# Performance work log

Hardware: AMD Instinct MI355X
Metric: run time of the kernel (lower is better)

The kernel has to match this reference:

```python
import jax, jax.numpy as jnp
import numpy as np

N, T, D, H = 64, 512, 512, 512


def setup_inputs() -> dict:
    key = jax.random.key(0)
    k1, k2, k3, k4 = jax.random.split(key, 4)
    x = jax.random.normal(k1, (N, T, D), dtype=jnp.float32)
    h0 = jax.random.normal(k2, (N, H), dtype=jnp.float32)
    Wx = jax.random.normal(k3, (D, H), dtype=jnp.float32) / jnp.sqrt(jnp.float32(D))
    Wh = jax.random.normal(k4, (H, H), dtype=jnp.float32) / jnp.sqrt(jnp.float32(H))
    b = jnp.zeros((H,), dtype=jnp.float32)
    return {"x": x, "h0": h0, "Wx": Wx, "Wh": Wh, "b": b}


def reference(x, h0, Wx, Wh, b):
    # Precompute the input-to-hidden projection for all timesteps at once
    # (one big GEMM), then scan the sequential hidden-state recurrence.
    xWx = jnp.einsum('ntd,dh->nth', x, Wx) + b  # (N, T, H)

    def step(h_prev, xw_t):
        h_next = jnp.tanh(xw_t + h_prev @ Wh)  # (N, H)
        return h_next, h_next

    # scan over time: move T to leading axis
    _, h_seq = jax.lax.scan(step, h0, jnp.swapaxes(xWx, 0, 1))  # (T, N, H)
    return jnp.swapaxes(h_seq, 0, 1)  # (N, T, H)
```

## Files before the change

kernel.cpp:

```cpp
#include <hip/hip_runtime.h>
#include <hip/hip_bf16.h>
#include <cmath>


#define DH     512
#define NSEQ   64
#define TSTEPS 512
#define MTOT   32768

typedef float v2f __attribute__((ext_vector_type(2)));

__global__ __launch_bounds__(256) void xw_gemm(
    const float* __restrict__ X,
    const float* __restrict__ Wx,
    const float* __restrict__ b,
    float* __restrict__ XW)
{
    __shared__ float As[16][64];
    __shared__ float Bs[16][64];

    const int bm = blockIdx.x * 64;
    const int bn = blockIdx.y * 64;
    const int tid = threadIdx.x;
    const int tr = tid >> 4;
    const int tc = tid & 15;

    float acc[4][4] = {};

    for (int k0 = 0; k0 < DH; k0 += 16) {
        {
            int m  = tid >> 2;
            int kk = (tid & 3) * 4;
            const float4 v = *(const float4*)&X[(size_t)(bm + m) * DH + k0 + kk];
            As[kk + 0][m] = v.x; As[kk + 1][m] = v.y;
            As[kk + 2][m] = v.z; As[kk + 3][m] = v.w;
        }
        {
            int k  = tid >> 4;
            int j4 = (tid & 15) * 4;
            *(float4*)&Bs[k][j4] = *(const float4*)&Wx[(size_t)(k0 + k) * DH + bn + j4];
        }
        __syncthreads();

        #pragma unroll
        for (int k = 0; k < 16; ++k) {
            float a0 = As[k][tr * 4 + 0], a1 = As[k][tr * 4 + 1];
            float a2 = As[k][tr * 4 + 2], a3 = As[k][tr * 4 + 3];
            float b0 = Bs[k][tc * 4 + 0], b1 = Bs[k][tc * 4 + 1];
            float b2 = Bs[k][tc * 4 + 2], b3 = Bs[k][tc * 4 + 3];
            acc[0][0] += a0 * b0; acc[0][1] += a0 * b1; acc[0][2] += a0 * b2; acc[0][3] += a0 * b3;
            acc[1][0] += a1 * b0; acc[1][1] += a1 * b1; acc[1][2] += a1 * b2; acc[1][3] += a1 * b3;
            acc[2][0] += a2 * b0; acc[2][1] += a2 * b1; acc[2][2] += a2 * b2; acc[2][3] += a2 * b3;
            acc[3][0] += a3 * b0; acc[3][1] += a3 * b1; acc[3][2] += a3 * b2; acc[3][3] += a3 * b3;
        }
        __syncthreads();
    }

    #pragma unroll
    for (int i = 0; i < 4; ++i) {
        const size_t row = (size_t)(bm + tr * 4 + i);
        #pragma unroll
        for (int j = 0; j < 4; ++j) {
            const int col = bn + tc * 4 + j;
            XW[row * DH + col] = acc[i][j] + b[col];
        }
    }
}

__global__ __launch_bounds__(512, 2) void rnn_rec5(
    const float* __restrict__ Wh,
    const float* __restrict__ h0,
    float* __restrict__ out,
    unsigned long long* __restrict__ hbuf)
{
    __shared__ float hslice[8][64];
    __shared__ float partb[2][8][128];

    const int bid  = blockIdx.x;
    const int xcd  = bid & 7;
    const int idx  = bid >> 3;
    const int seq  = xcd * 8 + (idx & 7);
    const int part = idx >> 3;
    const int tid  = threadIdx.x;
    const int lane = tid & 63;
    const int s    = tid >> 6;
    const int colbase = part * 128;
    const int c0   = colbase + lane * 2;

    v2f wv[64];
    #pragma unroll
    for (int k = 0; k < 64; ++k)
        wv[k] = *(const v2f*)&Wh[(size_t)(s * 64 + k) * DH + c0];
    #pragma unroll
    for (int k = 0; k < 64; ++k)
        asm volatile("" : "+v"(wv[k]));

    const int rwave = s - 2 * part;
    const bool is_reducer = (rwave == 0) | (rwave == 1);
    const int q     = rwave * 64 + lane;
    const int mycol = colbase + q;
    const int slot  = s * 64 + lane;

    hslice[s][lane] = h0[(size_t)seq * DH + slot];

    float* __restrict__ outn = out + (size_t)seq * TSTEPS * DH;
    float xw_cur = is_reducer ? outn[mycol] : 0.0f;

    for (int t = 0; t < TSTEPS; ++t) {
        const int buf = t & 1;

        v2f acc = {0.0f, 0.0f};
        #pragma unroll
        for (int qq = 0; qq < 16; ++qq) {
            const float4 h4 = *(const float4*)&hslice[s][qq * 4];
            v2f hb;
            hb.x = h4.x; hb.y = h4.x; acc = __builtin_elementwise_fma(hb, wv[4*qq+0], acc);
            hb.x = h4.y; hb.y = h4.y; acc = __builtin_elementwise_fma(hb, wv[4*qq+1], acc);
            hb.x = h4.z; hb.y = h4.z; acc = __builtin_elementwise_fma(hb, wv[4*qq+2], acc);
            hb.x = h4.w; hb.y = h4.w; acc = __builtin_elementwise_fma(hb, wv[4*qq+3], acc);
        }
        *(v2f*)&partb[buf][s][lane * 2] = acc;
        __syncthreads();

        unsigned long long* hb64 = &hbuf[((size_t)buf * NSEQ + seq) * DH];
        if (is_reducer) {
            float ssum = partb[buf][0][q] + partb[buf][1][q]
                       + partb[buf][2][q] + partb[buf][3][q]
                       + partb[buf][4][q] + partb[buf][5][q]
                       + partb[buf][6][q] + partb[buf][7][q];
            const float hval = tanhf(xw_cur + ssum);
            if (t < TSTEPS - 1) {
                const unsigned long long v =
                    ((unsigned long long)(unsigned)(t + 1) << 32) |
                    (unsigned long long)__float_as_uint(hval);
                __hip_atomic_store(&hb64[mycol], v,
                                   __ATOMIC_RELAXED, __HIP_MEMORY_SCOPE_AGENT);
            }
            hslice[s][lane] = hval;
            outn[(size_t)t * DH + mycol] = hval;
            if (t < TSTEPS - 1)
                xw_cur = outn[(size_t)(t + 1) * DH + mycol];
        } else if (t < TSTEPS - 1) {
            unsigned long long v;
            do {
                v = __hip_atomic_load(&hb64[slot], __ATOMIC_RELAXED,
                                      __HIP_MEMORY_SCOPE_AGENT);
            } while ((unsigned)(v >> 32) < (unsigned)(t + 1));
            hslice[s][lane] = __uint_as_float((unsigned)v);
        }
    }
}

__global__ __launch_bounds__(1024) void rnn_rec(
    const float* __restrict__ Wh,
    const float* __restrict__ h0,
    float* __restrict__ out)
{
    __shared__ float hsh[DH];
    __shared__ float part[8][DH];

    const int n     = blockIdx.x;
    const int tid   = threadIdx.x;
    const int jgrp  = tid & 127;
    const int ks    = tid >> 7;
    const int kbase = ks * 64;

    if (tid < DH) hsh[tid] = h0[(size_t)n * DH + tid];
    __syncthreads();

    const float4* __restrict__ Wh4 = (const float4*)Wh;
    float* __restrict__ outn = out + (size_t)n * TSTEPS * DH;

    float xw_cur = (tid < DH) ? outn[tid] : 0.0f;

    for (int t = 0; t < TSTEPS; ++t) {
        float xw_next = 0.0f;
        if (tid < DH && t < TSTEPS - 1) xw_next = outn[(size_t)(t + 1) * DH + tid];

        float4 acc = {0.0f, 0.0f, 0.0f, 0.0f};
        #pragma unroll 8
        for (int k = 0; k < 64; ++k) {
            const float hk = hsh[kbase + k];
            const float4 w = Wh4[(size_t)(kbase + k) * 128 + jgrp];
            acc.x += hk * w.x; acc.y += hk * w.y;
            acc.z += hk * w.z; acc.w += hk * w.w;
        }
        *(float4*)&part[ks][jgrp * 4] = acc;
        __syncthreads();

        if (tid < DH) {
            const int j = tid;
            float sum = part[0][j] + part[1][j] + part[2][j] + part[3][j]
                      + part[4][j] + part[5][j] + part[6][j] + part[7][j];
            const float hv = tanhf(xw_cur + sum);
            hsh[j] = hv;
            outn[(size_t)t * DH + j] = hv;
            xw_cur = xw_next;
        }
        __syncthreads();
    }
}

extern "C" void kernel_launch(void* const* d_in, const int* in_sizes, int n_in,
                              void* d_out, int out_size, void* d_ws, size_t ws_size,
                              hipStream_t stream) {
    const float* x  = (const float*)d_in[0];
    const float* h0 = (const float*)d_in[1];
    const float* Wx = (const float*)d_in[2];
    const float* Wh = (const float*)d_in[3];
    const float* b  = (const float*)d_in[4];
    float* out = (float*)d_out;

    xw_gemm<<<dim3(MTOT / 64, DH / 64), 256, 0, stream>>>(x, Wx, b, out);

    const size_t hbuf_bytes = (size_t)2 * NSEQ * DH * sizeof(unsigned long long);
    if (ws_size >= hbuf_bytes) {
        unsigned long long* hbuf = (unsigned long long*)d_ws;
        hipMemsetAsync(hbuf, 0, hbuf_bytes, stream);
        rnn_rec5<<<256, 512, 0, stream>>>(Wh, h0, out, hbuf);
    } else {
        rnn_rec<<<NSEQ, 1024, 0, stream>>>(Wh, h0, out);
    }
}
```

Measured before the change: 890.8 us.

## Interleave two sequences per block to hide cross-block hidden-state exchange latency

Each block now handles two sequences (a column quarter of each) instead of one, halving the grid to 128 blocks. The two sequences' steps are interleaved, and the polling load for one sequence's exchanged hidden state is issued before the other sequence's matvec runs, so global-memory exchange latency overlaps with compute. The block-to-sequence mapping also drops the XCD-aware grouping, so the blocks exchanging data for a sequence may no longer share an XCD. That can raise cross-die atomic latency, and two barriers per step add serialization.

```diff
diff --git a/kernel.cpp b/kernel.cpp
--- a/kernel.cpp
+++ b/kernel.cpp
@@ -67,20 +67,20 @@
     }
 }
 
-__global__ __launch_bounds__(512, 2) void rnn_rec5(
+__global__ __launch_bounds__(512, 2) void rnn_rec7(
     const float* __restrict__ Wh,
     const float* __restrict__ h0,
     float* __restrict__ out,
     unsigned long long* __restrict__ hbuf)
 {
-    __shared__ float hslice[8][64];
+    __shared__ float hslice[2][8][64];
     __shared__ float partb[2][8][128];
 
     const int bid  = blockIdx.x;
-    const int xcd  = bid & 7;
-    const int idx  = bid >> 3;
-    const int seq  = xcd * 8 + (idx & 7);
-    const int part = idx >> 3;
+    const int part = bid & 3;
+    const int g    = bid >> 2;
+    const int seq0 = g * 2;
+    const int seq1 = seq0 + 1;
     const int tid  = threadIdx.x;
     const int lane = tid & 63;
     const int s    = tid >> 6;
@@ -101,52 +101,113 @@
     const int mycol = colbase + q;
     const int slot  = s * 64 + lane;
 
-    hslice[s][lane] = h0[(size_t)seq * DH + slot];
-
-    float* __restrict__ outn = out + (size_t)seq * TSTEPS * DH;
-    float xw_cur = is_reducer ? outn[mycol] : 0.0f;
+    hslice[0][s][lane] = h0[(size_t)seq0 * DH + slot];
+    hslice[1][s][lane] = h0[(size_t)seq1 * DH + slot];
+
+    float* __restrict__ o0 = out + (size_t)seq0 * TSTEPS * DH;
+    float* __restrict__ o1 = out + (size_t)seq1 * TSTEPS * DH;
+    float xw0 = is_reducer ? o0[mycol] : 0.0f;
+    float xw1 = is_reducer ? o1[mycol] : 0.0f;
+
+    unsigned long long* const b0s0 = &hbuf[((size_t)0 * NSEQ + seq0) * DH];
+    unsigned long long* const b1s0 = &hbuf[((size_t)1 * NSEQ + seq0) * DH];
+    unsigned long long* const b0s1 = &hbuf[((size_t)0 * NSEQ + seq1) * DH];
+    unsigned long long* const b1s1 = &hbuf[((size_t)1 * NSEQ + seq1) * DH];
+
+    unsigned long long pf0 = 0, pf1 = 0;
+    __syncthreads();
 
     for (int t = 0; t < TSTEPS; ++t) {
         const int buf = t & 1;
-
-        v2f acc = {0.0f, 0.0f};
-        #pragma unroll
-        for (int qq = 0; qq < 16; ++qq) {
-            const float4 h4 = *(const float4*)&hslice[s][qq * 4];
-            v2f hb;
-            hb.x = h4.x; hb.y = h4.x; acc = __builtin_elementwise_fma(hb, wv[4*qq+0], acc);
-            hb.x = h4.y; hb.y = h4.y; acc = __builtin_elementwise_fma(hb, wv[4*qq+1], acc);
-            hb.x = h4.z; hb.y = h4.z; acc = __builtin_elementwise_fma(hb, wv[4*qq+2], acc);
-            hb.x = h4.w; hb.y = h4.w; acc = __builtin_elementwise_fma(hb, wv[4*qq+3], acc);
-        }
-        *(v2f*)&partb[buf][s][lane * 2] = acc;
-        __syncthreads();
-
-        unsigned long long* hb64 = &hbuf[((size_t)buf * NSEQ + seq) * DH];
+        const unsigned wantP = (unsigned)t;
+        unsigned long long* const pb0 = buf ? b0s0 : b1s0;
+        unsigned long long* const pb1 = buf ? b0s1 : b1s1;
+        unsigned long long* const cb0 = buf ? b1s0 : b0s0;
+        unsigned long long* const cb1 = buf ? b1s1 : b0s1;
+
+        if (t > 0 && !is_reducer) {
+            pf1 = __hip_atomic_load(&pb1[slot], __ATOMIC_RELAXED,
+                                    __HIP_MEMORY_SCOPE_AGENT);
+            unsigned long long v = pf0;
+            while ((unsigned)(v >> 32) < wantP)
+                v = __hip_atomic_load(&pb0[slot], __ATOMIC_RELAXED,
+                                      __HIP_MEMORY_SCOPE_AGENT);
+            hslice[0][s][lane] = __uint_as_float((unsigned)v);
+        }
+
+        {
+            v2f acc = {0.0f, 0.0f};
+            #pragma unroll
+            for (int qq = 0; qq < 16; ++qq) {
+                const float4 h4 = *(const float4*)&hslice[0][s][qq * 4];
+                v2f hb;
+                hb.x = h4.x; hb.y = h4.x; acc = __builtin_elementwise_fma(hb, wv[4*qq+0], acc);
+                hb.x = h4.y; hb.y = h4.y; acc = __builtin_elementwise_fma(hb, wv[4*qq+1], acc);
+                hb.x = h4.z; hb.y = h4.z; acc = __builtin_elementwise_fma(hb, wv[4*qq+2], acc);
+                hb.x = h4.w; hb.y = h4.w; acc = __builtin_elementwise_fma(hb, wv[4*qq+3], acc);
+            }
+            *(v2f*)&partb[0][s][lane * 2] = acc;
+        }
+        __syncthreads();
+
         if (is_reducer) {
-            float ssum = partb[buf][0][q] + partb[buf][1][q]
-                       + partb[buf][2][q] + partb[buf][3][q]
-                       + partb[buf][4][q] + partb[buf][5][q]
-                       + partb[buf][6][q] + partb[buf][7][q];
-            const float hval = tanhf(xw_cur + ssum);
+            float ssum = partb[0][0][q] + partb[0][1][q] + partb[0][2][q] + partb[0][3][q]
+                       + partb[0][4][q] + partb[0][5][q] + partb[0][6][q] + partb[0][7][q];
+            const float hv = tanhf(xw0 + ssum);
             if (t < TSTEPS - 1) {
                 const unsigned long long v =
                     ((unsigned long long)(unsigned)(t + 1) << 32) |
-                    (unsigned long long)__float_as_uint(hval);
-                __hip_atomic_store(&hb64[mycol], v,
+                    (unsigned long long)__float_as_uint(hv);
+                __hip_atomic_store(&cb0[mycol], v,
                                    __ATOMIC_RELAXED, __HIP_MEMORY_SCOPE_AGENT);
             }
-            hslice[s][lane] = hval;
-            outn[(size_t)t * DH + mycol] = hval;
+            hslice[0][s][lane] = hv;
+            o0[(size_t)t * DH + mycol] = hv;
             if (t < TSTEPS - 1)
-                xw_cur = outn[(size_t)(t + 1) * DH + mycol];
+                xw0 = o0[(size_t)(t + 1) * DH + mycol];
         } else if (t < TSTEPS - 1) {
-            unsigned long long v;
-            do {
-                v = __hip_atomic_load(&hb64[slot], __ATOMIC_RELAXED,
+            pf0 = __hip_atomic_load(&cb0[slot], __ATOMIC_RELAXED,
+                                    __HIP_MEMORY_SCOPE_AGENT);
+        }
+
+        if (t > 0 && !is_reducer) {
+            unsigned long long v = pf1;
+            while ((unsigned)(v >> 32) < wantP)
+                v = __hip_atomic_load(&pb1[slot], __ATOMIC_RELAXED,
                                       __HIP_MEMORY_SCOPE_AGENT);
-            } while ((unsigned)(v >> 32) < (unsigned)(t + 1));
-            hslice[s][lane] = __uint_as_float((unsigned)v);
+            hslice[1][s][lane] = __uint_as_float((unsigned)v);
+        }
+
+        {
+            v2f acc = {0.0f, 0.0f};
+            #pragma unroll
+            for (int qq = 0; qq < 16; ++qq) {
+                const float4 h4 = *(const float4*)&hslice[1][s][qq * 4];
+                v2f hb;
+                hb.x = h4.x; hb.y = h4.x; acc = __builtin_elementwise_fma(hb, wv[4*qq+0], acc);
+                hb.x = h4.y; hb.y = h4.y; acc = __builtin_elementwise_fma(hb, wv[4*qq+1], acc);
+                hb.x = h4.z; hb.y = h4.z; acc = __builtin_elementwise_fma(hb, wv[4*qq+2], acc);
+                hb.x = h4.w; hb.y = h4.w; acc = __builtin_elementwise_fma(hb, wv[4*qq+3], acc);
+            }
+            *(v2f*)&partb[1][s][lane * 2] = acc;
+        }
+        __syncthreads();
+
+        if (is_reducer) {
+            float ssum = partb[1][0][q] + partb[1][1][q] + partb[1][2][q] + partb[1][3][q]
+                       + partb[1][4][q] + partb[1][5][q] + partb[1][6][q] + partb[1][7][q];
+            const float hv = tanhf(xw1 + ssum);
+            if (t < TSTEPS - 1) {
+                const unsigned long long v =
+                    ((unsigned long long)(unsigned)(t + 1) << 32) |
+                    (unsigned long long)__float_as_uint(hv);
+                __hip_atomic_store(&cb1[mycol], v,
+                                   __ATOMIC_RELAXED, __HIP_MEMORY_SCOPE_AGENT);
+            }
+            hslice[1][s][lane] = hv;
+            o1[(size_t)t * DH + mycol] = hv;
+            if (t < TSTEPS - 1)
+                xw1 = o1[(size_t)(t + 1) * DH + mycol];
         }
     }
 }
@@ -217,7 +278,7 @@
     if (ws_size >= hbuf_bytes) {
         unsigned long long* hbuf = (unsigned long long*)d_ws;
         hipMemsetAsync(hbuf, 0, hbuf_bytes, stream);
-        rnn_rec5<<<256, 512, 0, stream>>>(Wh, h0, out, hbuf);
+        rnn_rec7<<<128, 512, 0, stream>>>(Wh, h0, out, hbuf);
     } else {
         rnn_rec<<<NSEQ, 1024, 0, stream>>>(Wh, h0, out);
     }
```

After: 1.340 ms. 50.5% more time.

## Split recurrence by K-slices with per-column owner reduction via global flags

Applied to the files above, without the earlier changes.

Adds a new recurrent kernel in which each of the four blocks per sequence holds a 128-row K-slice of Wh in registers and computes a partial dot product for all 512 columns. Non-owner threads publish their partials through tagged 64-bit atomic slots, and the owning block spins on three slots, sums them, applies tanh and stores its 128-element h piece. Compared with the previous kernel, each block now needs only its own h slice plus three remote partials per column, removing the full-h broadcast and the cross-wave LDS reduction. The cost is three polled global loads per owner thread per step and a workspace three times larger. It is used when the workspace is large enough, and the older kernels stay as fallbacks.

```diff
diff --git a/kernel.cpp b/kernel.cpp
--- a/kernel.cpp
+++ b/kernel.cpp
@@ -67,6 +67,96 @@
     }
 }
 
+__global__ __launch_bounds__(512, 2) void rnn_rec9(
+    const float* __restrict__ Wh,
+    const float* __restrict__ h0,
+    float* __restrict__ out,
+    unsigned long long* __restrict__ hbuf)
+{
+    __shared__ float hpiece[2][128];
+
+    const int bid  = blockIdx.x;
+    const int xcd  = bid & 7;
+    const int idx  = bid >> 3;
+    const int seq  = xcd * 8 + (idx & 7);
+    const int part = idx >> 3;
+    const int tid  = threadIdx.x;
+    const int kbase = part * 128;
+
+    float wv[128];
+    #pragma unroll
+    for (int kk = 0; kk < 128; ++kk)
+        wv[kk] = Wh[(size_t)(kbase + kk) * DH + tid];
+    #pragma unroll
+    for (int kk = 0; kk < 128; ++kk)
+        asm volatile("" : "+v"(wv[kk]));
+
+    const int  pj       = tid >> 7;
+    const bool is_owner = (pj == part);
+    const int  isl      = part - (part > pj ? 1 : 0);
+
+    if (tid < 128) hpiece[0][tid] = h0[(size_t)seq * DH + kbase + tid];
+
+    float* __restrict__ outn = out + (size_t)seq * TSTEPS * DH;
+    float xw_cur    = is_owner ? outn[tid] : 0.0f;
+    float hval_prev = 0.0f;
+
+    unsigned long long* const sb0 = hbuf + ((size_t)(0 * NSEQ + seq) * DH + tid) * 3;
+    unsigned long long* const sb1 = hbuf + ((size_t)(1 * NSEQ + seq) * DH + tid) * 3;
+
+    __syncthreads();
+
+    for (int t = 0; t < TSTEPS; ++t) {
+        const int buf = t & 1;
+        const float* hp = hpiece[buf];
+
+        float a0 = 0.0f, a1 = 0.0f, a2 = 0.0f, a3 = 0.0f;
+        #pragma unroll
+        for (int kk = 0; kk < 128; kk += 4) {
+            const float4 h4 = *(const float4*)&hp[kk];
+            a0 = fmaf(h4.x, wv[kk + 0], a0);
+            a1 = fmaf(h4.y, wv[kk + 1], a1);
+            a2 = fmaf(h4.z, wv[kk + 2], a2);
+            a3 = fmaf(h4.w, wv[kk + 3], a3);
+        }
+        const float contrib = (a0 + a1) + (a2 + a3);
+
+        unsigned long long* const sb = buf ? sb1 : sb0;
+        const unsigned want = (unsigned)(t + 1);
+
+        if (!is_owner) {
+            const unsigned long long v =
+                ((unsigned long long)want << 32) |
+                (unsigned long long)__float_as_uint(contrib);
+            __hip_atomic_store(sb + isl, v, __ATOMIC_RELAXED,
+                               __HIP_MEMORY_SCOPE_AGENT);
+        } else {
+            if (t > 0) outn[(size_t)(t - 1) * DH + tid] = hval_prev;
+            float xw_next = (t < TSTEPS - 1) ? outn[(size_t)(t + 1) * DH + tid]
+                                             : 0.0f;
+            unsigned long long v0, v1, v2;
+            do {
+                v0 = __hip_atomic_load(sb + 0, __ATOMIC_RELAXED,
+                                       __HIP_MEMORY_SCOPE_AGENT);
+                v1 = __hip_atomic_load(sb + 1, __ATOMIC_RELAXED,
+                                       __HIP_MEMORY_SCOPE_AGENT);
+                v2 = __hip_atomic_load(sb + 2, __ATOMIC_RELAXED,
+                                       __HIP_MEMORY_SCOPE_AGENT);
+            } while ((unsigned)(v0 >> 32) < want ||
+                     (unsigned)(v1 >> 32) < want ||
+                     (unsigned)(v2 >> 32) < want);
+            const float z = xw_cur
+                + ((contrib + __uint_as_float((unsigned)v0))
+                 + (__uint_as_float((unsigned)v1) + __uint_as_float((unsigned)v2)));
+            hval_prev = tanhf(z);
+            hpiece[buf ^ 1][tid & 127] = hval_prev;
+            xw_cur = xw_next;
+        }
+        __syncthreads();
+    }
+    if (is_owner) outn[(size_t)(TSTEPS - 1) * DH + tid] = hval_prev;
+}
+
 __global__ __launch_bounds__(512, 2) void rnn_rec5(
     const float* __restrict__ Wh,
     const float* __restrict__ h0,
@@ -108,7 +198,6 @@
 
     for (int t = 0; t < TSTEPS; ++t) {
         const int buf = t & 1;
-
         v2f acc = {0.0f, 0.0f};
         #pragma unroll
         for (int qq = 0; qq < 16; ++qq) {
@@ -213,10 +302,15 @@
 
     xw_gemm<<<dim3(MTOT / 64, DH / 64), 256, 0, stream>>>(x, Wx, b, out);
 
-    const size_t hbuf_bytes = (size_t)2 * NSEQ * DH * sizeof(unsigned long long);
-    if (ws_size >= hbuf_bytes) {
+    const size_t rec9_bytes = (size_t)2 * NSEQ * DH * 3 * sizeof(unsigned long long);
+    const size_t rec5_bytes = (size_t)2 * NSEQ * DH * sizeof(unsigned long long);
+    if (ws_size >= rec9_bytes) {
         unsigned long long* hbuf = (unsigned long long*)d_ws;
-        hipMemsetAsync(hbuf, 0, hbuf_bytes, stream);
+        hipMemsetAsync(hbuf, 0, rec9_bytes, stream);
+        rnn_rec9<<<256, 512, 0, stream>>>(Wh, h0, out, hbuf);
+    } else if (ws_size >= rec5_bytes) {
+        unsigned long long* hbuf = (unsigned long long*)d_ws;
+        hipMemsetAsync(hbuf, 0, rec5_bytes, stream);
         rnn_rec5<<<256, 512, 0, stream>>>(Wh, h0, out, hbuf);
     } else {
         rnn_rec<<<NSEQ, 1024, 0, stream>>>(Wh, h0, out);
```

Result: slower. 1.683 ms (+88.9%).

## Fuse input projection GEMM into recurrent kernel, computing xW tiles during spin-waits

Applied to the files above, without the earlier changes.

Removes the separate xw_gemm launch when workspace is available. The recurrent kernel now computes the x·Wx projection for its own sequence and column slice in 64-timestep tiles held in shared memory, one 8-wide k-chunk per recurrence step, while waiting for peers' hidden states. This is meant to hide GEMM work in the latency-bound recurrence and to avoid writing and re-reading the projection through global memory. In exchange it adds shared memory, register pressure and extra work on the per-step critical path, which could lengthen each step.

```diff
diff --git a/kernel.cpp b/kernel.cpp
--- a/kernel.cpp
+++ b/kernel.cpp
@@ -10,71 +10,49 @@
 
 typedef float v2f __attribute__((ext_vector_type(2)));
 
-__global__ __launch_bounds__(256) void xw_gemm(
+#define GEMM_CHUNK(SB)                                                         \
+    {                                                                          \
+        float2 w2[8];                                                          \
+        _Pragma("unroll")                                                      \
+        for (int kk = 0; kk < 8; ++kk)                                         \
+            w2[kk] = *(const float2*)&wstage[SB][kk][gc * 2];                  \
+        _Pragma("unroll")                                                      \
+        for (int r = 0; r < 8; ++r) {                                          \
+            const float4 xa = *(const float4*)&xstage[SB][rg * 8 + r][0];      \
+            const float4 xb = *(const float4*)&xstage[SB][rg * 8 + r][4];      \
+            accg[r][0] = fmaf(xa.x, w2[0].x, accg[r][0]);                      \
+            accg[r][1] = fmaf(xa.x, w2[0].y, accg[r][1]);                      \
+            accg[r][0] = fmaf(xa.y, w2[1].x, accg[r][0]);                      \
+            accg[r][1] = fmaf(xa.y, w2[1].y, accg[r][1]);                      \
+            accg[r][0] = fmaf(xa.z, w2[2].x, accg[r][0]);                      \
+            accg[r][1] = fmaf(xa.z, w2[2].y, accg[r][1]);                      \
+            accg[r][0] = fmaf(xa.w, w2[3].x, accg[r][0]);                      \
+            accg[r][1] = fmaf(xa.w, w2[3].y, accg[r][1]);                      \
+            accg[r][0] = fmaf(xb.x, w2[4].x, accg[r][0]);                      \
+            accg[r][1] = fmaf(xb.x, w2[4].y, accg[r][1]);                      \
+            accg[r][0] = fmaf(xb.y, w2[5].x, accg[r][0]);                      \
+            accg[r][1] = fmaf(xb.y, w2[5].y, accg[r][1]);                      \
+            accg[r][0] = fmaf(xb.z, w2[6].x, accg[r][0]);                      \
+            accg[r][1] = fmaf(xb.z, w2[6].y, accg[r][1]);                      \
+            accg[r][0] = fmaf(xb.w, w2[7].x, accg[r][0]);                      \
+            accg[r][1] = fmaf(xb.w, w2[7].y, accg[r][1]);                      \
+        }                                                                      \
+    }
+
+__global__ __launch_bounds__(512, 2) void rnn_fused2(
     const float* __restrict__ X,
     const float* __restrict__ Wx,
-    const float* __restrict__ b,
-    float* __restrict__ XW)
-{
-    __shared__ float As[16][64];
-    __shared__ float Bs[16][64];
-
-    const int bm = blockIdx.x * 64;
-    const int bn = blockIdx.y * 64;
-    const int tid = threadIdx.x;
-    const int tr = tid >> 4;
-    const int tc = tid & 15;
-
-    float acc[4][4] = {};
-
-    for (int k0 = 0; k0 < DH; k0 += 16) {
-        {
-            int m  = tid >> 2;
-            int kk = (tid & 3) * 4;
-            const float4 v = *(const float4*)&X[(size_t)(bm + m) * DH + k0 + kk];
-            As[kk + 0][m] = v.x; As[kk + 1][m] = v.y;
-            As[kk + 2][m] = v.z; As[kk + 3][m] = v.w;
-        }
-        {
-            int k  = tid >> 4;
-            int j4 = (tid & 15) * 4;
-            *(float4*)&Bs[k][j4] = *(const float4*)&Wx[(size_t)(k0 + k) * DH + bn + j4];
-        }
-        __syncthreads();
-
-        #pragma unroll
-        for (int k = 0; k < 16; ++k) {
-            float a0 = As[k][tr * 4 + 0], a1 = As[k][tr * 4 + 1];
-            float a2 = As[k][tr * 4 + 2], a3 = As[k][tr * 4 + 3];
-            float b0 = Bs[k][tc * 4 + 0], b1 = Bs[k][tc * 4 + 1];
-            float b2 = Bs[k][tc * 4 + 2], b3 = Bs[k][tc * 4 + 3];
-            acc[0][0] += a0 * b0; acc[0][1] += a0 * b1; acc[0][2] += a0 * b2; acc[0][3] += a0 * b3;
-            acc[1][0] += a1 * b0; acc[1][1] += a1 * b1; acc[1][2] += a1 * b2; acc[1][3] += a1 * b3;
-            acc[2][0] += a2 * b0; acc[2][1] += a2 * b1; acc[2][2] += a2 * b2; acc[2][3] += a2 * b3;
-            acc[3][0] += a3 * b0; acc[3][1] += a3 * b1; acc[3][2] += a3 * b2; acc[3][3] += a3 * b3;
-        }
-        __syncthreads();
-    }
-
-    #pragma unroll
-    for (int i = 0; i < 4; ++i) {
-        const size_t row = (size_t)(bm + tr * 4 + i);
-        #pragma unroll
-        for (int j = 0; j < 4; ++j) {
-            const int col = bn + tc * 4 + j;
-            XW[row * DH + col] = acc[i][j] + b[col];
-        }
-    }
-}
-
-__global__ __launch_bounds__(512, 2) void rnn_rec5(
+    const float* __restrict__ bias,
     const float* __restrict__ Wh,
     const float* __restrict__ h0,
     float* __restrict__ out,
     unsigned long long* __restrict__ hbuf)
 {
+    __shared__ float xwtile[2][64][128];
     __shared__ float hslice[8][64];
     __shared__ float partb[2][8][128];
+    __shared__ float xstage[2][64][8];
+    __shared__ float wstage[2][8][128];
 
     const int bid  = blockIdx.x;
     const int xcd  = bid & 7;
@@ -102,12 +80,44 @@
     const int slot  = s * 64 + lane;
 
     hslice[s][lane] = h0[(size_t)seq * DH + slot];
+    const float bias_r = is_reducer ? bias[mycol] : 0.0f;
 
     float* __restrict__ outn = out + (size_t)seq * TSTEPS * DH;
-    float xw_cur = is_reducer ? outn[mycol] : 0.0f;
+    const float* __restrict__ Xn = X + (size_t)seq * TSTEPS * DH;
+
+    const int gc  = lane;
+    const int rg  = s;
+    const int sxr = tid >> 3, sxk = tid & 7;
+    const int swk = tid >> 6, swc = tid & 63;
+
+    float accg[8][2];
+    #pragma unroll
+    for (int r = 0; r < 8; ++r) { accg[r][0] = 0.0f; accg[r][1] = 0.0f; }
+
+    for (int u = 0; u < 64; ++u) {
+        const float  pxv = Xn[(size_t)sxr * DH + u * 8 + sxk];
+        const float2 pwv = *(const float2*)&Wx[(size_t)(u * 8 + swk) * DH + colbase + swc * 2];
+        xstage[u & 1][sxr][sxk] = pxv;
+        *(float2*)&wstage[u & 1][swk][swc * 2] = pwv;
+        __syncthreads();
+        GEMM_CHUNK(u & 1);
+    }
+    #pragma unroll
+    for (int r = 0; r < 8; ++r) {
+        float2 v; v.x = accg[r][0]; v.y = accg[r][1];
+        *(float2*)&xwtile[0][rg * 8 + r][gc * 2] = v;
+        accg[r][0] = 0.0f; accg[r][1] = 0.0f;
+    }
+    __syncthreads();
+
+    float  pxv = Xn[(size_t)(64 + sxr) * DH + sxk];
+    float2 pwv = *(const float2*)&Wx[(size_t)swk * DH + colbase + swc * 2];
 
     for (int t = 0; t < TSTEPS; ++t) {
         const int buf = t & 1;
+        const int tb  = (t >> 6) + 1;
+        const int u   = t & 63;
+        const bool building = (tb < 8);
 
         v2f acc = {0.0f, 0.0f};
         #pragma unroll
@@ -120,15 +130,21 @@
             hb.x = h4.w; hb.y = h4.w; acc = __builtin_elementwise_fma(hb, wv[4*qq+3], acc);
         }
         *(v2f*)&partb[buf][s][lane * 2] = acc;
+
+        if (building) {
+            xstage[buf][sxr][sxk] = pxv;
+            *(float2*)&wstage[buf][swk][swc * 2] = pwv;
+        }
         __syncthreads();
 
         unsigned long long* hb64 = &hbuf[((size_t)buf * NSEQ + seq) * DH];
         if (is_reducer) {
+            const float xwv = xwtile[(t >> 6) & 1][u][q] + bias_r;
             float ssum = partb[buf][0][q] + partb[buf][1][q]
                        + partb[buf][2][q] + partb[buf][3][q]
                        + partb[buf][4][q] + partb[buf][5][q]
                        + partb[buf][6][q] + partb[buf][7][q];
-            const float hval = tanhf(xw_cur + ssum);
+            const float hval = tanhf(xwv + ssum);
             if (t < TSTEPS - 1) {
                 const unsigned long long v =
                     ((unsigned long long)(unsigned)(t + 1) << 32) |
@@ -138,9 +154,28 @@
             }
             hslice[s][lane] = hval;
             outn[(size_t)t * DH + mycol] = hval;
-            if (t < TSTEPS - 1)
-                xw_cur = outn[(size_t)(t + 1) * DH + mycol];
-        } else if (t < TSTEPS - 1) {
+        }
+
+        if (building && t < 447) {
+            const int tb2 = ((t + 1) >> 6) + 1;
+            const int u2  = (t + 1) & 63;
+            pxv = Xn[(size_t)(tb2 * 64 + sxr) * DH + u2 * 8 + sxk];
+            pwv = *(const float2*)&Wx[(size_t)(u2 * 8 + swk) * DH + colbase + swc * 2];
+        }
+
+        if (building) {
+            GEMM_CHUNK(buf);
+            if (u == 63) {
+                #pragma unroll
+                for (int r = 0; r < 8; ++r) {
+                    float2 v; v.x = accg[r][0]; v.y = accg[r][1];
+                    *(float2*)&xwtile[tb & 1][rg * 8 + r][gc * 2] = v;
+                    accg[r][0] = 0.0f; accg[r][1] = 0.0f;
+                }
+            }
+        }
+
+        if (!is_reducer && t < TSTEPS - 1) {
             unsigned long long v;
             do {
                 v = __hip_atomic_load(&hb64[slot], __ATOMIC_RELAXED,
@@ -151,50 +186,73 @@
     }
 }
 
+__global__ __launch_bounds__(256) void xw_gemm(
+    const float* __restrict__ X, const float* __restrict__ Wx,
+    const float* __restrict__ b, float* __restrict__ XW)
+{
+    __shared__ float As[16][64];
+    __shared__ float Bs[16][64];
+    const int bm = blockIdx.x * 64, bn = blockIdx.y * 64;
+    const int tid = threadIdx.x, tr = tid >> 4, tc = tid & 15;
+    float acc[4][4] = {};
+    for (int k0 = 0; k0 < DH; k0 += 16) {
+        { int m = tid >> 2, kk = (tid & 3) * 4;
+          const float4 v = *(const float4*)&X[(size_t)(bm + m) * DH + k0 + kk];
+          As[kk][m]=v.x; As[kk+1][m]=v.y; As[kk+2][m]=v.z; As[kk+3][m]=v.w; }
+        { int k = tid >> 4, j4 = (tid & 15) * 4;
+          *(float4*)&Bs[k][j4] = *(const float4*)&Wx[(size_t)(k0 + k) * DH + bn + j4]; }
+        __syncthreads();
+        #pragma unroll
+        for (int k = 0; k < 16; ++k) {
+            float a0=As[k][tr*4],a1=As[k][tr*4+1],a2=As[k][tr*4+2],a3=As[k][tr*4+3];
+            float b0=Bs[k][tc*4],b1=Bs[k][tc*4+1],b2=Bs[k][tc*4+2],b3=Bs[k][tc*4+3];
+            acc[0][0]+=a0*b0;acc[0][1]+=a0*b1;acc[0][2]+=a0*b2;acc[0][3]+=a0*b3;
+            acc[1][0]+=a1*b0;acc[1][1]+=a1*b1;acc[1][2]+=a1*b2;acc[1][3]+=a1*b3;
+            acc[2][0]+=a2*b0;acc[2][1]+=a2*b1;acc[2][2]+=a2*b2;acc[2][3]+=a2*b3;
+            acc[3][0]+=a3*b0;acc[3][1]+=a3*b1;acc[3][2]+=a3*b2;acc[3][3]+=a3*b3;
+        }
+        __syncthreads();
+    }
+    #pragma unroll
+    for (int i = 0; i < 4; ++i) {
+        const size_t row = (size_t)(bm + tr * 4 + i);
+        #pragma unroll
+        for (int j = 0; j < 4; ++j)
+            XW[row * DH + bn + tc * 4 + j] = acc[i][j] + b[bn + tc * 4 + j];
+    }
+}
+
 __global__ __launch_bounds__(1024) void rnn_rec(
-    const float* __restrict__ Wh,
-    const float* __restrict__ h0,
+    const float* __restrict__ Wh, const float* __restrict__ h0,
     float* __restrict__ out)
 {
     __shared__ float hsh[DH];
     __shared__ float part[8][DH];
-
-    const int n     = blockIdx.x;
-    const int tid   = threadIdx.x;
-    const int jgrp  = tid & 127;
-    const int ks    = tid >> 7;
-    const int kbase = ks * 64;
-
+    const int n = blockIdx.x, tid = threadIdx.x;
+    const int jgrp = tid & 127, ks = tid >> 7, kbase = ks * 64;
     if (tid < DH) hsh[tid] = h0[(size_t)n * DH + tid];
     __syncthreads();
-
     const float4* __restrict__ Wh4 = (const float4*)Wh;
     float* __restrict__ outn = out + (size_t)n * TSTEPS * DH;
-
     float xw_cur = (tid < DH) ? outn[tid] : 0.0f;
-
     for (int t = 0; t < TSTEPS; ++t) {
         float xw_next = 0.0f;
         if (tid < DH && t < TSTEPS - 1) xw_next = outn[(size_t)(t + 1) * DH + tid];
-
-        float4 acc = {0.0f, 0.0f, 0.0f, 0.0f};
+        float4 acc = {0,0,0,0};
         #pragma unroll 8
         for (int k = 0; k < 64; ++k) {
             const float hk = hsh[kbase + k];
             const float4 w = Wh4[(size_t)(kbase + k) * 128 + jgrp];
-            acc.x += hk * w.x; acc.y += hk * w.y;
-            acc.z += hk * w.z; acc.w += hk * w.w;
+            acc.x += hk*w.x; acc.y += hk*w.y; acc.z += hk*w.z; acc.w += hk*w.w;
         }
         *(float4*)&part[ks][jgrp * 4] = acc;
         __syncthreads();
-
         if (tid < DH) {
-            const int j = tid;
-            float sum = part[0][j] + part[1][j] + part[2][j] + part[3][j]
-                      + part[4][j] + part[5][j] + part[6][j] + part[7][j];
+            float sum = part[0][tid]+part[1][tid]+part[2][tid]+part[3][tid]
+                      + part[4][tid]+part[5][tid]+part[6][tid]+part[7][tid];
             const float hv = tanhf(xw_cur + sum);
-            hsh[j] = hv;
-            outn[(size_t)t * DH + j] = hv;
+            hsh[tid] = hv;
+            outn[(size_t)t * DH + tid] = hv;
             xw_cur = xw_next;
         }
         __syncthreads();
@@ -211,14 +269,13 @@
     const float* b  = (const float*)d_in[4];
     float* out = (float*)d_out;
 
-    xw_gemm<<<dim3(MTOT / 64, DH / 64), 256, 0, stream>>>(x, Wx, b, out);
-
     const size_t hbuf_bytes = (size_t)2 * NSEQ * DH * sizeof(unsigned long long);
     if (ws_size >= hbuf_bytes) {
         unsigned long long* hbuf = (unsigned long long*)d_ws;
         hipMemsetAsync(hbuf, 0, hbuf_bytes, stream);
-        rnn_rec5<<<256, 512, 0, stream>>>(Wh, h0, out, hbuf);
+        rnn_fused2<<<256, 512, 0, stream>>>(x, Wx, b, Wh, h0, out, hbuf);
     } else {
+        xw_gemm<<<dim3(MTOT / 64, DH / 64), 256, 0, stream>>>(x, Wx, b, out);
         rnn_rec<<<NSEQ, 1024, 0, stream>>>(Wh, h0, out);
     }
 }
```

Measured after the change: 787.9 us, median of 2. -11.6%, faster.
